# Kernel tuning notes

Measured on AMD Instinct MI355X. Metric: run time of the kernel, lower is better.

Reference implementation:

```python
import jax, jax.numpy as jnp
import numpy as np

NUM_JOINTS = 33
EPS = 1e-5
# MediaPipe 33-landmark pose skeleton connections
SKELETON_EDGES = np.array([
    [0,1],[1,2],[2,3],[3,7],[0,4],[4,5],[5,6],[6,8],[9,10],
    [11,12],[11,13],[13,15],[15,17],[15,19],[15,21],[17,19],
    [12,14],[14,16],[16,18],[16,20],[16,22],[18,20],
    [11,23],[12,24],[23,24],[23,25],[24,26],[25,27],[26,28],
    [27,29],[28,30],[29,31],[30,32],[27,31],[28,32]], dtype=np.int64)


def _batched_edges(B):
    und = np.concatenate([SKELETON_EDGES, SKELETON_EDGES[:, ::-1]], axis=0)
    loops = np.stack([np.arange(NUM_JOINTS)] * 2, axis=1)
    e = np.concatenate([und, loops], axis=0)  # [103, 2] per graph (incl. self loops)
    eb = (e[None, :, :] + (np.arange(B) * NUM_JOINTS)[:, None, None]).reshape(-1, 2)
    return jnp.asarray(eb[:, 0], dtype=jnp.int32), jnp.asarray(eb[:, 1], dtype=jnp.int32)


def setup_inputs() -> dict:
    key = jax.random.key(0)
    B, N, F, H, L = 4096, NUM_JOINTS, 256, 256, 4
    ks = jax.random.split(key, 20)
    d = {"x": jax.random.normal(ks[0], (B, N, F), dtype=jnp.float32)}
    dims = [(F, H), (H, H), (H, H)]
    i = 1
    for li, (di, do) in enumerate(dims):
        d[f"w{li}"] = jax.random.normal(ks[i], (di, do), dtype=jnp.float32) * 0.05; i += 1
        d[f"b{li}"] = jnp.zeros((do,), dtype=jnp.float32)
        d[f"g{li}"] = jnp.ones((do,), dtype=jnp.float32)
        d[f"be{li}"] = jnp.zeros((do,), dtype=jnp.float32)
    d["wh"] = jax.random.normal(ks[i], (H, H), dtype=jnp.float32) * 0.05; i += 1
    d["bh"] = jnp.zeros((H,), dtype=jnp.float32)
    d["wc"] = jax.random.normal(ks[i], (H, L), dtype=jnp.float32) * 0.05; i += 1
    d["bc"] = jnp.zeros((L,), dtype=jnp.float32)
    src, dst = _batched_edges(B)
    d["src"], d["dst"] = src, dst
    return d


def _gcn_conv(x, W, b, src, dst, norm, num_nodes):
    h = x @ W                          # [NN, out]
    msg = h[src] * norm[:, None]       # gather + scale
    agg = jax.ops.segment_sum(msg, dst, num_segments=num_nodes)
    return agg + b


def _bn_relu(x, g, be):
    mu = jnp.mean(x, axis=0)
    var = jnp.mean((x - mu) ** 2, axis=0)  # biased, torch training BN
    return jax.nn.relu((x - mu) * jax.lax.rsqrt(var + EPS) * g + be)


def reference(x, w0, b0, g0, be0, w1, b1, g1, be1, w2, b2, g2, be2, wh, bh, wc, bc, src, dst):
    B, N, F = x.shape
    NN = B * N
    h = jnp.nan_to_num(x.reshape(NN, F))
    # symmetric GCN normalization D^{-1/2}(A+I)D^{-1/2}; self loops already in edge list
    deg = jax.ops.segment_sum(jnp.ones_like(src, dtype=h.dtype), dst, num_segments=NN)
    dinv = jax.lax.rsqrt(deg)
    norm = dinv[src] * dinv[dst]
    for W, b, g, be in ((w0, b0, g0, be0), (w1, b1, g1, be1), (w2, b2, g2, be2)):
        h = _gcn_conv(h, W, b, src, dst, norm, NN)
        h = _bn_relu(h, g, be)  # dropout: eval mode -> identity
    h = _gcn_conv(h, wh, bh, src, dst, norm, NN)
    pooled = h.reshape(B, N, -1).mean(axis=1)  # global mean pool per graph
    return pooled @ wc + bc
```

## Files before the change

kernel.cpp:

```cpp
#include <hip/hip_runtime.h>

typedef unsigned short u16;
typedef __attribute__((ext_vector_type(8))) short short8;
typedef __attribute__((ext_vector_type(4))) float floatx4;

#define NN_TOT 135168

#define WAITVM(N) asm volatile("s_waitcnt vmcnt(" #N ")" ::: "memory")
#define WAITLGKM0 asm volatile("s_waitcnt lgkmcnt(0)" ::: "memory")
#define VMFENCE   asm volatile("" ::: "memory")

static constexpr int NBCNT[33] = {2,2,2,2,2,2,2,1,1,1,1,3,3,2,2,4,4,2,2,2,2,1,1,3,3,2,2,3,3,2,2,2,2};
static constexpr int NBR[33][4] = {
 {1,4,0,0},{0,2,0,0},{1,3,0,0},{2,7,0,0},{0,5,0,0},{4,6,0,0},{5,8,0,0},
 {3,0,0,0},{6,0,0,0},{10,0,0,0},{9,0,0,0},
 {12,13,23,0},{11,14,24,0},{11,15,0,0},{12,16,0,0},
 {13,17,19,21},{14,18,20,22},
 {15,19,0,0},{16,20,0,0},{15,17,0,0},{16,18,0,0},{15,0,0,0},{16,0,0,0},
 {11,24,25,0},{12,23,26,0},{23,27,0,0},{24,28,0,0},
 {25,29,31,0},{26,30,32,0},{27,31,0,0},{28,32,0,0},{29,27,0,0},{30,28,0,0}};
static constexpr float R2 = 0.70710678f, R3 = 0.57735027f, R4 = 0.5f, R5 = 0.44721360f;
static constexpr float DINV[33] = {R3,R3,R3,R3,R3,R3,R3, R2,R2,R2,R2, R4,R4, R3,R3, R5,R5,
                                   R3,R3,R3,R3, R2,R2, R4,R4, R3,R3, R4,R4, R3,R3,R3,R3};

__device__ __forceinline__ float bf2f(u16 u) {
  unsigned int v = ((unsigned int)u) << 16; float f; __builtin_memcpy(&f, &v, 4); return f;
}
__device__ __forceinline__ u16 f2bf(float f) {
  unsigned int u; __builtin_memcpy(&u, &f, 4);
  return (u16)((u + 0x7fffu + ((u >> 16) & 1u)) >> 16);
}
__device__ __forceinline__ float ldin(const void* p, int i, int isbf) {
  return isbf ? bf2f(((const u16*)p)[i]) : ((const float*)p)[i];
}
__device__ __forceinline__ void gload_lds16(const u16* g, u16* l) {
  __builtin_amdgcn_global_load_lds((const __attribute__((address_space(1))) unsigned int*)g,
                                   (__attribute__((address_space(3))) unsigned int*)l, 16, 0, 0);
}
__device__ __forceinline__ int lof(int row, int qq) {
  return row*32 + ((qq ^ ((row >> 1) & 3)) * 8);
}

__global__ __launch_bounds__(256) void detect_kernel(const u16* __restrict__ x,
                                                     int* __restrict__ flag)
{
  __shared__ int cnt[256];
  const int t = threadIdx.x;
  int c = 0;
  for (int j = 0; j < 16; ++j) {
    u16 u = x[(t*16 + j)*2];
    int e = (u >> 7) & 0xFF;
    c += (e >= 118 && e <= 130) ? 1 : 0;
  }
  cnt[t] = c;
  __syncthreads();
  if (t == 0) {
    int s = 0;
    for (int i = 0; i < 256; ++i) s += cnt[i];
    *flag = (s > 2048) ? 1 : 0;
  }
}

__global__ __launch_bounds__(256) void transpose_kernel(const void* __restrict__ w0,
    const void* __restrict__ w1, const void* __restrict__ w2, u16* __restrict__ Wt,
    const int* __restrict__ flag)
{
  const int m = blockIdx.x >> 4;
  const int nb = (blockIdx.x & 15) * 16;
  const void* W = m == 0 ? w0 : (m == 1 ? w1 : w2);
  u16* O = Wt + (size_t)m * 65536;
  const int t = threadIdx.x;
  const int lane = t & 63, wv = t >> 6;
  const int isbf = *flag;
  if (isbf) {
    const u16* Wb = (const u16*)W;
#pragma unroll
    for (int nn = 0; nn < 4; ++nn) {
      const int n = nb + nn*4 + wv;
#pragma unroll
      for (int j = 0; j < 4; ++j) {
        const int k = lane + 64*j;
        O[n*256 + k] = Wb[k*256 + n];
      }
    }
  } else {
    const float* Wf = (const float*)W;
#pragma unroll
    for (int nn = 0; nn < 4; ++nn) {
      const int n = nb + nn*4 + wv;
#pragma unroll
      for (int j = 0; j < 4; ++j) {
        const int k = lane + 64*j;
        O[n*256 + k] = f2bf(Wf[k*256 + n]);
      }
    }
  }
}

__global__ __launch_bounds__(256) void init_kernel(const void* __restrict__ wh,
    const void* __restrict__ bh, const void* __restrict__ wc, const void* __restrict__ bc,
    float* __restrict__ wq, float* __restrict__ bq, float* __restrict__ repl,
    const int* __restrict__ flag)
{
  const int idx = blockIdx.x*256 + threadIdx.x;
  for (int i = idx; i < 3*64*512; i += 65*256) repl[i] = 0.f;
  const int isbf = *flag;
  const int t = threadIdx.x;
  const int lane = t & 63;
  if (blockIdx.x < 64) {
    const int r = blockIdx.x*4 + (t >> 6);
    float a0=0.f, a1=0.f, a2=0.f, a3=0.f;
#pragma unroll
    for (int j = 0; j < 4; ++j) {
      const int k = lane + 64*j;
      const float w = ldin(wh, r*256 + k, isbf);
      a0 += w*ldin(wc, k*4+0, isbf); a1 += w*ldin(wc, k*4+1, isbf);
      a2 += w*ldin(wc, k*4+2, isbf); a3 += w*ldin(wc, k*4+3, isbf);
    }
#pragma unroll
    for (int off = 32; off; off >>= 1) {
      a0 += __shfl_xor(a0, off); a1 += __shfl_xor(a1, off);
      a2 += __shfl_xor(a2, off); a3 += __shfl_xor(a3, off);
    }
    if (lane == 0) { wq[r*4+0]=a0; wq[r*4+1]=a1; wq[r*4+2]=a2; wq[r*4+3]=a3; }
  } else if (t < 64) {
    float s0=0.f, s1=0.f, s2=0.f, s3=0.f;
#pragma unroll
    for (int j = 0; j < 4; ++j) {
      const int k = lane + 64*j;
      const float b = ldin(bh, k, isbf);
      s0 += b*ldin(wc, k*4+0, isbf); s1 += b*ldin(wc, k*4+1, isbf);
      s2 += b*ldin(wc, k*4+2, isbf); s3 += b*ldin(wc, k*4+3, isbf);
    }
#pragma unroll
    for (int off = 32; off; off >>= 1) {
      s0 += __shfl_xor(s0, off); s1 += __shfl_xor(s1, off);
      s2 += __shfl_xor(s2, off); s3 += __shfl_xor(s3, off);
    }
    if (lane == 0) {
      bq[0] = s0 + ldin(bc, 0, isbf); bq[1] = s1 + ldin(bc, 1, isbf);
      bq[2] = s2 + ldin(bc, 2, isbf); bq[3] = s3 + ldin(bc, 3, isbf);
    }
  }
}

template<int ACT>
__global__ __launch_bounds__(256, 2) void fused_kernel(
    const void* __restrict__ Ag, const u16* __restrict__ Bt,
    const float* __restrict__ fscale, const float* __restrict__ fshift,
    const void* __restrict__ bias, u16* __restrict__ H,
    float* __restrict__ repl, const int* __restrict__ flag)
{
  __shared__ __align__(16) u16 smem[25184];
  const int tid = threadIdx.x;
  const int lane = tid & 63, w = tid >> 6;
  const int gi = w >> 1, h = w & 1;
  const int fr = lane & 15, q = lane >> 4;
  const int lr = lane >> 2, cq = lane & 3;
  const int swz = (lr >> 1) & 3;
  const int r0 = tid >> 2;
  const int c8 = (tid & 3) * 8;
  const size_t R0 = (size_t)blockIdx.x * 66;
  const int dtf = *flag;
  const int isbf = (ACT == 0) ? dtf : 1;
  const u16* Ab = (const u16*)Ag;
  const float* Af = (const float*)Ag;
  float* const sS = (float*)(smem + 24160);

  floatx4 acc[3][8];
#pragma unroll
  for (int t = 0; t < 3; ++t)
#pragma unroll
    for (int j = 0; j < 8; ++j) acc[t][j] = (floatx4){0.f, 0.f, 0.f, 0.f};

  auto sAbuf = [&](int i) -> u16* { return smem + i*2592; };
  auto sBbuf = [&](int i) -> u16* { return smem + 7776 + i*8192; };

  auto issueB = [&](int t) {
    u16* dst = sBbuf(t & 1);
    const int k0 = t * 32;
#pragma unroll
    for (int i = 0; i < 4; ++i)
      gload_lds16(Bt + (w*64 + i*16 + lr)*256 + k0 + (cq ^ swz)*8,
                  dst + (w*64 + i*16)*32);
  };
  auto issueA_dma = [&](int t) {
    u16* dst = sAbuf(t % 3);
    const int k0 = t * 32;
    gload_lds16(Ab + (R0 + w*16 + lr)*256 + k0 + (cq ^ swz)*8, dst + (w*16)*32);
    if (w == 0) {
      size_t rg = R0 + 64 + lr;
      if (rg >= NN_TOT) rg = NN_TOT - 1;
      gload_lds16(Ab + rg*256 + k0 + (cq ^ swz)*8, dst + 64*32);
    }
  };

  uint4 regA[2], regA2[2];
  auto issueA_reg = [&](int t) {
    const int k0 = t * 32;
    regA[t & 1] = *(const uint4*)(Ab + (R0 + r0)*256 + k0 + c8);
    if (tid >= 248)
      regA2[t & 1] = *(const uint4*)(Ab + (R0 + 64 + ((tid - 248) >> 2))*256 + k0 + c8);
  };
  auto writeA = [&](int t) {
    u16* dst = sAbuf(t & 1);
    const int k0 = t * 32;
    const float4 s0 = *(const float4*)(sS + k0 + c8);
    const float4 s1 = *(const float4*)(sS + k0 + c8 + 4);
    const float4 t0 = *(const float4*)(sS + 256 + k0 + c8);
    const float4 t1 = *(const float4*)(sS + 256 + k0 + c8 + 4);
    const float sc[8] = {s0.x,s0.y,s0.z,s0.w, s1.x,s1.y,s1.z,s1.w};
    const float sh[8] = {t0.x,t0.y,t0.z,t0.w, t1.x,t1.y,t1.z,t1.w};
    {
      const u16* us = (const u16*)&regA[t & 1];
      u16 ov[8];
#pragma unroll
      for (int j = 0; j < 8; ++j)
        ov[j] = f2bf(fmaxf(0.f, fmaf(bf2f(us[j]), sc[j], sh[j])));
      *(uint4*)(dst + r0*32 + ((cq ^ ((r0 >> 1) & 3))*8)) = *(const uint4*)ov;
    }
    if (tid >= 248) {
      const int rr = 64 + ((tid - 248) >> 2);
      const u16* us = (const u16*)&regA2[t & 1];
      u16 ov[8];
#pragma unroll
      for (int j = 0; j < 8; ++j)
        ov[j] = f2bf(fmaxf(0.f, fmaf(bf2f(us[j]), sc[j], sh[j])));
      *(uint4*)(dst + rr*32 + ((cq ^ ((rr >> 1) & 3))*8)) = *(const uint4*)ov;
    }
  };

  auto computeP = [&](const u16* cA, const u16* cB) {
    short8 a[3], b[8];
#pragma unroll
    for (int t = 0; t < 3; ++t)
      a[t] = *(const short8*)(cA + lof(gi*33 + t*16 + fr, q));
#pragma unroll
    for (int nf = 0; nf < 8; ++nf)
      b[nf] = *(const short8*)(cB + lof(h*128 + nf*16 + fr, q));
#pragma unroll
    for (int t = 0; t < 3; ++t)
#pragma unroll
      for (int nf = 0; nf < 8; ++nf)
        acc[t][nf] = __builtin_amdgcn_mfma_f32_16x16x32_bf16(a[t], b[nf], acc[t][nf], 0, 0, 0);
  };

  if (ACT == 0 && !isbf) {
    for (int kc = 0; kc < 8; ++kc) {
      const int k0 = kc * 32;
      __syncthreads();
      {
        const float* ap = Af + (R0 + r0)*256 + k0 + c8;
        float4 p0 = *(const float4*)(ap);
        float4 p1 = *(const float4*)(ap + 4);
        u16 ov[8];
        ov[0]=f2bf(p0.x); ov[1]=f2bf(p0.y); ov[2]=f2bf(p0.z); ov[3]=f2bf(p0.w);
        ov[4]=f2bf(p1.x); ov[5]=f2bf(p1.y); ov[6]=f2bf(p1.z); ov[7]=f2bf(p1.w);
        *(uint4*)(sAbuf(0) + r0*32 + ((cq ^ ((r0 >> 1) & 3))*8)) = *(const uint4*)ov;
      }
      if (tid < 8) {
        const int rr = 64 + (tid >> 2);
        const float* ap = Af + (R0 + rr)*256 + k0 + c8;
        float4 p0 = *(const float4*)(ap);
        float4 p1 = *(const float4*)(ap + 4);
        u16 ov[8];
        ov[0]=f2bf(p0.x); ov[1]=f2bf(p0.y); ov[2]=f2bf(p0.z); ov[3]=f2bf(p0.w);
        ov[4]=f2bf(p1.x); ov[5]=f2bf(p1.y); ov[6]=f2bf(p1.z); ov[7]=f2bf(p1.w);
        *(uint4*)(sAbuf(0) + rr*32 + ((cq ^ ((rr >> 1) & 3))*8)) = *(const uint4*)ov;
      }
#pragma unroll
      for (int i = 0; i < 4; ++i)
        gload_lds16(Bt + (w*64 + i*16 + lr)*256 + k0 + (cq ^ swz)*8,
                    sBbuf(0) + (w*64 + i*16)*32);
      __syncthreads();
      computeP(sAbuf(0), sBbuf(0));
    }
  } else {
    if (ACT == 1) {
      const float f0 = fscale[tid], f1 = fshift[tid];
      WAITVM(0);
      sS[tid] = f0; sS[256 + tid] = f1;
      WAITLGKM0;
    }
    issueB(0);
    VMFENCE;
    if (ACT == 0) { issueA_dma(0); issueA_dma(1); }
    else          { issueA_reg(0); issueA_reg(1); }
    if (ACT == 1) {
      __builtin_amdgcn_s_barrier();
      writeA(0);
      WAITLGKM0;
    }
    const bool sp = (ACT == 0) ? (w == 0) : (w == 3);
#pragma unroll
    for (int kc = 0; kc < 8; ++kc) {
      if (kc < 7) issueB(kc + 1);
      VMFENCE;
      if (kc < 6) { if (ACT == 0) issueA_dma(kc + 2); else issueA_reg(kc + 2); }
      if (kc < 6)       { if (sp) { WAITVM(8); } else { WAITVM(6); } }
      else if (kc == 6) { if (sp) { WAITVM(6); } else { WAITVM(5); } }
      else              { WAITVM(0); }
      __builtin_amdgcn_sched_barrier(0);
      __builtin_amdgcn_s_barrier();
      computeP(ACT == 0 ? sAbuf(kc % 3) : sAbuf(kc & 1), sBbuf(kc & 1));
      if (ACT == 1 && kc < 7) {
        writeA(kc + 1);
        WAITLGKM0;
      }
    }
  }

  __syncthreads();
  u16* const Tl = smem;
#pragma unroll
  for (int t = 0; t < 3; ++t)
#pragma unroll
    for (int nf = 0; nf < 8; ++nf)
#pragma unroll
      for (int r = 0; r < 4; ++r) {
        const int row = t*16 + q*4 + r;
        if (row < 33)
          Tl[(gi*33 + row)*264 + h*128 + nf*16 + fr] = f2bf(acc[t][nf][r]);
      }
  __syncthreads();

  const int g2 = tid >> 7, cp = tid & 127;
  const size_t Gg = (size_t)blockIdx.x*2 + g2;
  float a0[33], a1[33];
#pragma unroll
  for (int d = 0; d < 33; ++d) { a0[d] = 0.f; a1[d] = 0.f; }
#pragma unroll
  for (int s = 0; s < 33; ++s) {
    const unsigned int pk = *(const unsigned int*)(Tl + (g2*33 + s)*264 + cp*2);
    const float v0 = bf2f((u16)(pk & 0xffffu)) * DINV[s];
    const float v1 = bf2f((u16)(pk >> 16)) * DINV[s];
    a0[s] += v0; a1[s] += v1;
#pragma unroll
    for (int i = 0; i < NBCNT[s]; ++i) { a0[NBR[s][i]] += v0; a1[NBR[s][i]] += v1; }
  }
  const float bv0 = ldin(bias, cp*2,     dtf);
  const float bv1 = ldin(bias, cp*2 + 1, dtf);
  float s10 = 0.f, s20 = 0.f, s11 = 0.f, s21 = 0.f;
  u16* hg = H + Gg * (33*256);
#pragma unroll
  for (int d = 0; d < 33; ++d) {
    const float o0 = fmaf(a0[d], DINV[d], bv0);
    const float o1 = fmaf(a1[d], DINV[d], bv1);
    const unsigned int pw = (unsigned int)f2bf(o0) | ((unsigned int)f2bf(o1) << 16);
    *(unsigned int*)(hg + d*256 + cp*2) = pw;
    s10 += o0; s20 += o0*o0; s11 += o1; s21 += o1*o1;
  }
  float* r1p = repl + (Gg & 63)*512;
  atomicAdd(r1p + cp*2,           s10);
  atomicAdd(r1p + cp*2 + 1,       s11);
  atomicAdd(r1p + 256 + cp*2,     s20);
  atomicAdd(r1p + 256 + cp*2 + 1, s21);
}

__global__ __launch_bounds__(256) void statfin_kernel(const float* __restrict__ repl,
    const void* __restrict__ gamma, const void* __restrict__ beta, float* __restrict__ fs,
    const int* __restrict__ flag)
{
  const int c = threadIdx.x;
  const int isbf = *flag;
  float s1 = 0.f, s2 = 0.f;
  for (int r = 0; r < 64; ++r) { s1 += repl[r*512 + c]; s2 += repl[r*512 + 256 + c]; }
  const float inv = 1.f / (float)NN_TOT;
  const float mu = s1 * inv;
  const float var = s2 * inv - mu*mu;
  const float rs = rsqrtf(var + 1e-5f);
  const float sc = rs * ldin(gamma, c, isbf);
  fs[c] = sc;
  fs[256 + c] = ldin(beta, c, isbf) - mu * sc;
}

__global__ __launch_bounds__(256) void final_kernel(const u16* __restrict__ H,
    const float* __restrict__ fs, const float* __restrict__ wq,
    const float* __restrict__ bq, void* __restrict__ outp,
    const int* __restrict__ flag)
{
  const int tid = threadIdx.x;
  const int lane = tid & 63, wv = tid >> 6;
  const size_t g = (size_t)blockIdx.x * 4 + wv;
  const int isbf = *flag;
  const int c4 = lane * 4;
  const float4 scv = *(const float4*)(fs + c4);
  const float4 shv = *(const float4*)(fs + 256 + c4);
  const u16* hg = H + g * (33*256);
  float v0 = 0.f, v1 = 0.f, v2 = 0.f, v3 = 0.f;
#pragma unroll
  for (int s = 0; s < 33; ++s) {
    float a = DINV[s];
#pragma unroll
    for (int i = 0; i < NBCNT[s]; ++i) a += DINV[NBR[s][i]];
    const float ws = DINV[s] * a * (1.f/33.f);
    const uint2 pk = *(const uint2*)(hg + s*256 + c4);
    v0 += ws * fmaxf(0.f, fmaf(bf2f((u16)(pk.x & 0xffffu)), scv.x, shv.x));
    v1 += ws * fmaxf(0.f, fmaf(bf2f((u16)(pk.x >> 16)),     scv.y, shv.y));
    v2 += ws * fmaxf(0.f, fmaf(bf2f((u16)(pk.y & 0xffffu)), scv.z, shv.z));
    v3 += ws * fmaxf(0.f, fmaf(bf2f((u16)(pk.y >> 16)),     scv.w, shv.w));
  }
  const float4 q0 = *(const float4*)(wq + (c4+0)*4);
  const float4 q1 = *(const float4*)(wq + (c4+1)*4);
  const float4 q2 = *(const float4*)(wq + (c4+2)*4);
  const float4 q3 = *(const float4*)(wq + (c4+3)*4);
  float p0 = v0*q0.x + v1*q1.x + v2*q2.x + v3*q3.x;
  float p1 = v0*q0.y + v1*q1.y + v2*q2.y + v3*q3.y;
  float p2 = v0*q0.z + v1*q1.z + v2*q2.z + v3*q3.z;
  float p3 = v0*q0.w + v1*q1.w + v2*q2.w + v3*q3.w;
#pragma unroll
  for (int off = 32; off; off >>= 1) {
    p0 += __shfl_xor(p0, off); p1 += __shfl_xor(p1, off);
    p2 += __shfl_xor(p2, off); p3 += __shfl_xor(p3, off);
  }
  if (lane == 0) {
    if (isbf) {
      u16* o = (u16*)outp + g*4;
      o[0]=f2bf(p0+bq[0]); o[1]=f2bf(p1+bq[1]); o[2]=f2bf(p2+bq[2]); o[3]=f2bf(p3+bq[3]);
    } else {
      float* o = (float*)outp + g*4;
      o[0]=p0+bq[0]; o[1]=p1+bq[1]; o[2]=p2+bq[2]; o[3]=p3+bq[3];
    }
  }
}

extern "C" void kernel_launch(void* const* d_in, const int* in_sizes, int n_in,
                              void* d_out, int out_size, void* d_ws, size_t ws_size,
                              hipStream_t stream)
{
  const void* x   = d_in[0];
  const void* w0  = d_in[1];
  const void* b0  = d_in[2];
  const void* g0  = d_in[3];
  const void* be0 = d_in[4];
  const void* w1  = d_in[5];
  const void* b1  = d_in[6];
  const void* g1  = d_in[7];
  const void* be1 = d_in[8];
  const void* w2  = d_in[9];
  const void* b2  = d_in[10];
  const void* g2  = d_in[11];
  const void* be2 = d_in[12];
  const void* wh  = d_in[13];
  const void* bh  = d_in[14];
  const void* wc  = d_in[15];
  const void* bc  = d_in[16];

  char* ws = (char*)d_ws;
  float* wq   = (float*)(ws + 0);
  float* bq   = (float*)(ws + 4096);
  float* fs   = (float*)(ws + 4608);
  int*   flag = (int*)  (ws + 12288);
  float* repl = (float*)(ws + 16384);
  u16*   Wt   = (u16*)  (ws + 409600);
  u16*   A    = (u16*)  (ws + 802816);
  (void)in_sizes; (void)n_in; (void)out_size; (void)ws_size;

  detect_kernel<<<1, 256, 0, stream>>>((const u16*)x, flag);
  transpose_kernel<<<48, 256, 0, stream>>>(w0, w1, w2, Wt, flag);
  init_kernel<<<65, 256, 0, stream>>>(wh, bh, wc, bc, wq, bq, repl, flag);

  fused_kernel<0><<<2048, 256, 0, stream>>>(x, Wt, nullptr, nullptr, b0, A, repl, flag);
  statfin_kernel<<<1, 256, 0, stream>>>(repl, g0, be0, fs, flag);
  fused_kernel<1><<<2048, 256, 0, stream>>>(A, Wt + 65536, fs, fs + 256, b1, A, repl + 32768, flag);
  statfin_kernel<<<1, 256, 0, stream>>>(repl + 32768, g1, be1, fs + 512, flag);
  fused_kernel<1><<<2048, 256, 0, stream>>>(A, Wt + 131072, fs + 512, fs + 768, b2, A, repl + 65536, flag);
  statfin_kernel<<<1, 256, 0, stream>>>(repl + 65536, g2, be2, fs + 1024, flag);
  final_kernel<<<1024, 256, 0, stream>>>(A, fs + 1024, wq, bq, d_out, flag);
}
```

Measured before the change: 420.0 us.

## Double threads per block in fused GCN kernel and triple-buffer A/B loads

Each fused GCN layer block now runs 512 threads (8 waves) instead of 256, so each wave covers a quarter of the output columns and holds half as many accumulators. The B tiles become triple-buffered, the A prefetch depth drops from two stages to one, and the wait counts are adjusted to match. The aggregation epilogue now gives each thread one channel instead of two. The intent is more waves per CU and lower register pressure to hide memory latency, at the cost of larger shared memory, shallower A prefetch, and narrower 16-bit stores in the epilogue.

```diff
diff --git a/kernel.cpp b/kernel.cpp
--- a/kernel.cpp
+++ b/kernel.cpp
@@ -145,103 +145,86 @@
 }
 
 template<int ACT>
-__global__ __launch_bounds__(256, 2) void fused_kernel(
+__global__ __launch_bounds__(512, 4) void fused_kernel(
     const void* __restrict__ Ag, const u16* __restrict__ Bt,
     const float* __restrict__ fscale, const float* __restrict__ fshift,
     const void* __restrict__ bias, u16* __restrict__ H,
     float* __restrict__ repl, const int* __restrict__ flag)
 {
-  __shared__ __align__(16) u16 smem[25184];
+  __shared__ __align__(16) u16 smem[33376];
   const int tid = threadIdx.x;
   const int lane = tid & 63, w = tid >> 6;
-  const int gi = w >> 1, h = w & 1;
+  const int gi = w >> 2, h = w & 3;
   const int fr = lane & 15, q = lane >> 4;
   const int lr = lane >> 2, cq = lane & 3;
   const int swz = (lr >> 1) & 3;
-  const int r0 = tid >> 2;
-  const int c8 = (tid & 3) * 8;
   const size_t R0 = (size_t)blockIdx.x * 66;
   const int dtf = *flag;
   const int isbf = (ACT == 0) ? dtf : 1;
   const u16* Ab = (const u16*)Ag;
   const float* Af = (const float*)Ag;
-  float* const sS = (float*)(smem + 24160);
-
-  floatx4 acc[3][8];
+  float* const sS = (float*)(smem + 32352);
+
+  floatx4 acc[3][4];
 #pragma unroll
   for (int t = 0; t < 3; ++t)
 #pragma unroll
-    for (int j = 0; j < 8; ++j) acc[t][j] = (floatx4){0.f, 0.f, 0.f, 0.f};
+    for (int j = 0; j < 4; ++j) acc[t][j] = (floatx4){0.f, 0.f, 0.f, 0.f};
 
   auto sAbuf = [&](int i) -> u16* { return smem + i*2592; };
   auto sBbuf = [&](int i) -> u16* { return smem + 7776 + i*8192; };
 
+  auto issueA_dma = [&](int t) {
+    if (w < 5) {
+      u16* dst = sAbuf(t % 3);
+      size_t rowg = R0 + w*16 + lr;
+      const size_t rmax = R0 + 65;
+      if (rowg > rmax) rowg = rmax;
+      gload_lds16(Ab + rowg*256 + t*32 + (cq ^ swz)*8, dst + (w*16)*32);
+    }
+  };
+  uint4 regA;
+  auto issueA_reg = [&](int t) {
+    if (tid < 264)
+      regA = *(const uint4*)(Ab + (R0 + (tid >> 2))*256 + t*32 + (tid & 3)*8);
+  };
   auto issueB = [&](int t) {
-    u16* dst = sBbuf(t & 1);
-    const int k0 = t * 32;
-#pragma unroll
-    for (int i = 0; i < 4; ++i)
-      gload_lds16(Bt + (w*64 + i*16 + lr)*256 + k0 + (cq ^ swz)*8,
-                  dst + (w*64 + i*16)*32);
-  };
-  auto issueA_dma = [&](int t) {
-    u16* dst = sAbuf(t % 3);
-    const int k0 = t * 32;
-    gload_lds16(Ab + (R0 + w*16 + lr)*256 + k0 + (cq ^ swz)*8, dst + (w*16)*32);
-    if (w == 0) {
-      size_t rg = R0 + 64 + lr;
-      if (rg >= NN_TOT) rg = NN_TOT - 1;
-      gload_lds16(Ab + rg*256 + k0 + (cq ^ swz)*8, dst + 64*32);
-    }
-  };
-
-  uint4 regA[2], regA2[2];
-  auto issueA_reg = [&](int t) {
-    const int k0 = t * 32;
-    regA[t & 1] = *(const uint4*)(Ab + (R0 + r0)*256 + k0 + c8);
-    if (tid >= 248)
-      regA2[t & 1] = *(const uint4*)(Ab + (R0 + 64 + ((tid - 248) >> 2))*256 + k0 + c8);
+    u16* dst = sBbuf(t % 3);
+#pragma unroll
+    for (int i = 0; i < 2; ++i)
+      gload_lds16(Bt + (w*32 + i*16 + lr)*256 + t*32 + (cq ^ swz)*8,
+                  dst + (w*32 + i*16)*32);
   };
   auto writeA = [&](int t) {
-    u16* dst = sAbuf(t & 1);
-    const int k0 = t * 32;
-    const float4 s0 = *(const float4*)(sS + k0 + c8);
-    const float4 s1 = *(const float4*)(sS + k0 + c8 + 4);
-    const float4 t0 = *(const float4*)(sS + 256 + k0 + c8);
-    const float4 t1 = *(const float4*)(sS + 256 + k0 + c8 + 4);
-    const float sc[8] = {s0.x,s0.y,s0.z,s0.w, s1.x,s1.y,s1.z,s1.w};
-    const float sh[8] = {t0.x,t0.y,t0.z,t0.w, t1.x,t1.y,t1.z,t1.w};
-    {
-      const u16* us = (const u16*)&regA[t & 1];
+    if (tid < 264) {
+      const int row = tid >> 2, cc = tid & 3;
+      const float4 s0 = *(const float4*)(sS + t*32 + cc*8);
+      const float4 s1 = *(const float4*)(sS + t*32 + cc*8 + 4);
+      const float4 t0 = *(const float4*)(sS + 256 + t*32 + cc*8);
+      const float4 t1 = *(const float4*)(sS + 256 + t*32 + cc*8 + 4);
+      const float sc[8] = {s0.x,s0.y,s0.z,s0.w, s1.x,s1.y,s1.z,s1.w};
+      const float sh[8] = {t0.x,t0.y,t0.z,t0.w, t1.x,t1.y,t1.z,t1.w};
+      const u16* us = (const u16*)&regA;
       u16 ov[8];
 #pragma unroll
       for (int j = 0; j < 8; ++j)
         ov[j] = f2bf(fmaxf(0.f, fmaf(bf2f(us[j]), sc[j], sh[j])));
-      *(uint4*)(dst + r0*32 + ((cq ^ ((r0 >> 1) & 3))*8)) = *(const uint4*)ov;
-    }
-    if (tid >= 248) {
-      const int rr = 64 + ((tid - 248) >> 2);
-      const u16* us = (const u16*)&regA2[t & 1];
-      u16 ov[8];
-#pragma unroll
-      for (int j = 0; j < 8; ++j)
-        ov[j] = f2bf(fmaxf(0.f, fmaf(bf2f(us[j]), sc[j], sh[j])));
-      *(uint4*)(dst + rr*32 + ((cq ^ ((rr >> 1) & 3))*8)) = *(const uint4*)ov;
+      *(uint4*)(sAbuf(t % 3) + row*32 + ((cc ^ ((row >> 1) & 3))*8)) = *(const uint4*)ov;
     }
   };
 
   auto computeP = [&](const u16* cA, const u16* cB) {
-    short8 a[3], b[8];
+    short8 a[3], b[4];
 #pragma unroll
     for (int t = 0; t < 3; ++t)
       a[t] = *(const short8*)(cA + lof(gi*33 + t*16 + fr, q));
 #pragma unroll
-    for (int nf = 0; nf < 8; ++nf)
-      b[nf] = *(const short8*)(cB + lof(h*128 + nf*16 + fr, q));
+    for (int nf = 0; nf < 4; ++nf)
+      b[nf] = *(const short8*)(cB + lof(h*64 + nf*16 + fr, q));
 #pragma unroll
     for (int t = 0; t < 3; ++t)
 #pragma unroll
-      for (int nf = 0; nf < 8; ++nf)
+      for (int nf = 0; nf < 4; ++nf)
         acc[t][nf] = __builtin_amdgcn_mfma_f32_16x16x32_bf16(a[t], b[nf], acc[t][nf], 0, 0, 0);
   };
 
@@ -249,60 +232,49 @@
     for (int kc = 0; kc < 8; ++kc) {
       const int k0 = kc * 32;
       __syncthreads();
-      {
-        const float* ap = Af + (R0 + r0)*256 + k0 + c8;
+      if (tid < 264) {
+        const int row = tid >> 2, cc = tid & 3;
+        const float* ap = Af + (R0 + row)*256 + k0 + cc*8;
         float4 p0 = *(const float4*)(ap);
         float4 p1 = *(const float4*)(ap + 4);
         u16 ov[8];
         ov[0]=f2bf(p0.x); ov[1]=f2bf(p0.y); ov[2]=f2bf(p0.z); ov[3]=f2bf(p0.w);
         ov[4]=f2bf(p1.x); ov[5]=f2bf(p1.y); ov[6]=f2bf(p1.z); ov[7]=f2bf(p1.w);
-        *(uint4*)(sAbuf(0) + r0*32 + ((cq ^ ((r0 >> 1) & 3))*8)) = *(const uint4*)ov;
-      }
-      if (tid < 8) {
-        const int rr = 64 + (tid >> 2);
-        const float* ap = Af + (R0 + rr)*256 + k0 + c8;
-        float4 p0 = *(const float4*)(ap);
-        float4 p1 = *(const float4*)(ap + 4);
-        u16 ov[8];
-        ov[0]=f2bf(p0.x); ov[1]=f2bf(p0.y); ov[2]=f2bf(p0.z); ov[3]=f2bf(p0.w);
-        ov[4]=f2bf(p1.x); ov[5]=f2bf(p1.y); ov[6]=f2bf(p1.z); ov[7]=f2bf(p1.w);
-        *(uint4*)(sAbuf(0) + rr*32 + ((cq ^ ((rr >> 1) & 3))*8)) = *(const uint4*)ov;
-      }
-#pragma unroll
-      for (int i = 0; i < 4; ++i)
-        gload_lds16(Bt + (w*64 + i*16 + lr)*256 + k0 + (cq ^ swz)*8,
-                    sBbuf(0) + (w*64 + i*16)*32);
+        *(uint4*)(sAbuf(0) + row*32 + ((cc ^ ((row >> 1) & 3))*8)) = *(const uint4*)ov;
+      }
+#pragma unroll
+      for (int i = 0; i < 2; ++i)
+        gload_lds16(Bt + (w*32 + i*16 + lr)*256 + k0 + (cq ^ swz)*8,
+                    sBbuf(0) + (w*32 + i*16)*32);
       __syncthreads();
       computeP(sAbuf(0), sBbuf(0));
     }
   } else {
     if (ACT == 1) {
-      const float f0 = fscale[tid], f1 = fshift[tid];
-      WAITVM(0);
-      sS[tid] = f0; sS[256 + tid] = f1;
+      if (tid < 256) { const float f0 = fscale[tid], f1 = fshift[tid];
+                       sS[tid] = f0; sS[256 + tid] = f1; }
+    }
+    if (ACT == 0) issueA_dma(0); else issueA_reg(0);
+    VMFENCE;
+    issueB(0);
+    if (ACT == 1) {
       WAITLGKM0;
-    }
-    issueB(0);
-    VMFENCE;
-    if (ACT == 0) { issueA_dma(0); issueA_dma(1); }
-    else          { issueA_reg(0); issueA_reg(1); }
-    if (ACT == 1) {
       __builtin_amdgcn_s_barrier();
       writeA(0);
       WAITLGKM0;
     }
-    const bool sp = (ACT == 0) ? (w == 0) : (w == 3);
 #pragma unroll
     for (int kc = 0; kc < 8; ++kc) {
-      if (kc < 7) issueB(kc + 1);
-      VMFENCE;
-      if (kc < 6) { if (ACT == 0) issueA_dma(kc + 2); else issueA_reg(kc + 2); }
-      if (kc < 6)       { if (sp) { WAITVM(8); } else { WAITVM(6); } }
-      else if (kc == 6) { if (sp) { WAITVM(6); } else { WAITVM(5); } }
-      else              { WAITVM(0); }
+      if (kc < 7) {
+        if (ACT == 0) issueA_dma(kc + 1); else issueA_reg(kc + 1);
+        VMFENCE;
+        issueB(kc + 1);
+      }
+      if (kc < 7) { if (w < 5) { WAITVM(3); } else { WAITVM(2); } }
+      else        { WAITVM(0); }
       __builtin_amdgcn_sched_barrier(0);
       __builtin_amdgcn_s_barrier();
-      computeP(ACT == 0 ? sAbuf(kc % 3) : sAbuf(kc & 1), sBbuf(kc & 1));
+      computeP(sAbuf(kc % 3), sBbuf(kc % 3));
       if (ACT == 1 && kc < 7) {
         writeA(kc + 1);
         WAITLGKM0;
@@ -315,46 +287,39 @@
 #pragma unroll
   for (int t = 0; t < 3; ++t)
 #pragma unroll
-    for (int nf = 0; nf < 8; ++nf)
+    for (int nf = 0; nf < 4; ++nf)
 #pragma unroll
       for (int r = 0; r < 4; ++r) {
         const int row = t*16 + q*4 + r;
         if (row < 33)
-          Tl[(gi*33 + row)*264 + h*128 + nf*16 + fr] = f2bf(acc[t][nf][r]);
+          Tl[(gi*33 + row)*264 + h*64 + nf*16 + fr] = f2bf(acc[t][nf][r]);
       }
   __syncthreads();
 
-  const int g2 = tid >> 7, cp = tid & 127;
+  const int g2 = tid >> 8, c = tid & 255;
   const size_t Gg = (size_t)blockIdx.x*2 + g2;
-  float a0[33], a1[33];
-#pragma unroll
-  for (int d = 0; d < 33; ++d) { a0[d] = 0.f; a1[d] = 0.f; }
+  float a0[33];
+#pragma unroll
+  for (int d = 0; d < 33; ++d) a0[d] = 0.f;
 #pragma unroll
   for (int s = 0; s < 33; ++s) {
-    const unsigned int pk = *(const unsigned int*)(Tl + (g2*33 + s)*264 + cp*2);
-    const float v0 = bf2f((u16)(pk & 0xffffu)) * DINV[s];
-    const float v1 = bf2f((u16)(pk >> 16)) * DINV[s];
-    a0[s] += v0; a1[s] += v1;
-#pragma unroll
-    for (int i = 0; i < NBCNT[s]; ++i) { a0[NBR[s][i]] += v0; a1[NBR[s][i]] += v1; }
-  }
-  const float bv0 = ldin(bias, cp*2,     dtf);
-  const float bv1 = ldin(bias, cp*2 + 1, dtf);
-  float s10 = 0.f, s20 = 0.f, s11 = 0.f, s21 = 0.f;
+    const float v = bf2f(Tl[(g2*33 + s)*264 + c]) * DINV[s];
+    a0[s] += v;
+#pragma unroll
+    for (int i = 0; i < NBCNT[s]; ++i) a0[NBR[s][i]] += v;
+  }
+  const float bv = ldin(bias, c, dtf);
+  float s1 = 0.f, s2 = 0.f;
   u16* hg = H + Gg * (33*256);
 #pragma unroll
   for (int d = 0; d < 33; ++d) {
-    const float o0 = fmaf(a0[d], DINV[d], bv0);
-    const float o1 = fmaf(a1[d], DINV[d], bv1);
-    const unsigned int pw = (unsigned int)f2bf(o0) | ((unsigned int)f2bf(o1) << 16);
-    *(unsigned int*)(hg + d*256 + cp*2) = pw;
-    s10 += o0; s20 += o0*o0; s11 += o1; s21 += o1*o1;
+    const float o = fmaf(a0[d], DINV[d], bv);
+    hg[d*256 + c] = f2bf(o);
+    s1 += o; s2 += o*o;
   }
   float* r1p = repl + (Gg & 63)*512;
-  atomicAdd(r1p + cp*2,           s10);
-  atomicAdd(r1p + cp*2 + 1,       s11);
-  atomicAdd(r1p + 256 + cp*2,     s20);
-  atomicAdd(r1p + 256 + cp*2 + 1, s21);
+  atomicAdd(r1p + c,       s1);
+  atomicAdd(r1p + 256 + c, s2);
 }
 
 __global__ __launch_bounds__(256) void statfin_kernel(const float* __restrict__ repl,
@@ -460,11 +425,11 @@
   transpose_kernel<<<48, 256, 0, stream>>>(w0, w1, w2, Wt, flag);
   init_kernel<<<65, 256, 0, stream>>>(wh, bh, wc, bc, wq, bq, repl, flag);
 
-  fused_kernel<0><<<2048, 256, 0, stream>>>(x, Wt, nullptr, nullptr, b0, A, repl, flag);
+  fused_kernel<0><<<2048, 512, 0, stream>>>(x, Wt, nullptr, nullptr, b0, A, repl, flag);
   statfin_kernel<<<1, 256, 0, stream>>>(repl, g0, be0, fs, flag);
-  fused_kernel<1><<<2048, 256, 0, stream>>>(A, Wt + 65536, fs, fs + 256, b1, A, repl + 32768, flag);
+  fused_kernel<1><<<2048, 512, 0, stream>>>(A, Wt + 65536, fs, fs + 256, b1, A, repl + 32768, flag);
   statfin_kernel<<<1, 256, 0, stream>>>(repl + 32768, g1, be1, fs + 512, flag);
-  fused_kernel<1><<<2048, 256, 0, stream>>>(A, Wt + 131072, fs + 512, fs + 768, b2, A, repl + 65536, flag);
+  fused_kernel<1><<<2048, 512, 0, stream>>>(A, Wt + 131072, fs + 512, fs + 768, b2, A, repl + 65536, flag);
   statfin_kernel<<<1, 256, 0, stream>>>(repl + 65536, g2, be2, fs + 1024, flag);
   final_kernel<<<1024, 256, 0, stream>>>(A, fs + 1024, wq, bq, d_out, flag);
 }
```

New measurement: 395.7 us. -5.8%, faster.
